# Kernel optimization log

Measured on AMD Instinct MI355X. Metric: run time of the kernel, lower is better.

Reference implementation:

```python
import jax, jax.numpy as jnp
import numpy as np

B, T, D_IN, P, Q, D_OUT = 128, 1024, 64, 128, 2, 64


def _lstm_layer(x, w_ih, w_hh, b):
    """One LSTM layer, batch_first. x: [B,T,Din], w_ih: [4P,Din], w_hh: [4P,P], b: [4P].
    PyTorch gate order: i, f, g, o."""
    # Precompute input contribution for all timesteps (the big, parallel GEMM).
    gx = jnp.einsum('btd,gd->btg', x, w_ih) + b          # [B,T,4P]
    gx_t = jnp.swapaxes(gx, 0, 1)                        # [T,B,4P] for scan
    p = w_hh.shape[1]
    h0 = jnp.zeros((x.shape[0], p), dtype=x.dtype)
    c0 = jnp.zeros((x.shape[0], p), dtype=x.dtype)

    def step(carry, g_in):
        h, c = carry
        g = g_in + h @ w_hh.T                            # [B,4P]
        i, f, gg, o = jnp.split(g, 4, axis=-1)
        i = jax.nn.sigmoid(i)
        f = jax.nn.sigmoid(f)
        gg = jnp.tanh(gg)
        o = jax.nn.sigmoid(o)
        c = f * c + i * gg
        h = o * jnp.tanh(c)
        return (h, c), h

    _, hs = jax.lax.scan(step, (h0, c0), gx_t)           # hs: [T,B,P]
    return jnp.swapaxes(hs, 0, 1)                        # [B,T,P]


def setup_inputs() -> dict:
    key = jax.random.key(0)
    ks = jax.random.split(key, 8)
    x = jax.random.normal(ks[0], (B, T, D_IN), dtype=jnp.float32)
    # weight_ih: kaiming-normal-ish; weight_hh: orthogonal-ish (random normal is a fine stand-in
    # numerically; init distribution doesn't change the math being tested).
    w_ih0 = jax.random.normal(ks[1], (4 * P, D_IN), dtype=jnp.float32) * (1.0 / np.sqrt(D_IN))
    w_hh0 = jax.random.normal(ks[2], (4 * P, P), dtype=jnp.float32) * (1.0 / np.sqrt(P))
    w_ih1 = jax.random.normal(ks[3], (4 * P, P), dtype=jnp.float32) * (1.0 / np.sqrt(P))
    w_hh1 = jax.random.normal(ks[4], (4 * P, P), dtype=jnp.float32) * (1.0 / np.sqrt(P))
    # biases initialized to zero in the original (bias_ih + bias_hh folded into one per layer
    # would be equivalent math; keep both for faithfulness)
    b_ih = jnp.zeros((Q, 4 * P), dtype=jnp.float32)
    b_hh = jnp.zeros((Q, 4 * P), dtype=jnp.float32)
    fc_w = jax.random.normal(ks[5], (D_OUT, P), dtype=jnp.float32) * np.sqrt(2.0 / P)
    fc_b = jnp.zeros((D_OUT,), dtype=jnp.float32)
    return {"x": x, "w_ih0": w_ih0, "w_hh0": w_hh0, "w_ih1": w_ih1, "w_hh1": w_hh1,
            "b_ih": b_ih, "b_hh": b_hh, "fc_w": fc_w, "fc_b": fc_b}


def reference(x, w_ih0, w_hh0, w_ih1, w_hh1, b_ih, b_hh, fc_w, fc_b):
    h = _lstm_layer(x, w_ih0, w_hh0, b_ih[0] + b_hh[0])   # layer 0: [B,T,P]
    h = _lstm_layer(h, w_ih1, w_hh1, b_ih[1] + b_hh[1])   # layer 1: [B,T,P]
    return jnp.einsum('btp,op->bto', h, fc_w) + fc_b      # [B,T,D_OUT]
```

## Files before the change

### kernel.cpp

```cpp
#include <hip/hip_runtime.h>

#define NT 1024
#define H0S 256
#define GS 64
#define LAG 32

typedef _Float16 half8 __attribute__((ext_vector_type(8)));
typedef _Float16 half4 __attribute__((ext_vector_type(4)));
typedef float f32x4 __attribute__((ext_vector_type(4)));
typedef unsigned long long u64;

#ifndef __has_builtin
#define __has_builtin(x) 0
#endif

__device__ __forceinline__ f32x4 MFMA(half8 a, half8 b, f32x4 c) {
  return __builtin_amdgcn_mfma_f32_16x16x32_f16(a, b, c, 0, 0, 0);
}
__device__ __forceinline__ float exp2h(float x) {
#if __has_builtin(__builtin_amdgcn_exp2f)
  return __builtin_amdgcn_exp2f(x);
#else
  return exp2f(x);
#endif
}
__device__ __forceinline__ float sigf(float x) {
  return __builtin_amdgcn_rcpf(1.0f + exp2h(x * -1.44269504f));
}
__device__ __forceinline__ float tanhf2(float x) {
  float t = __builtin_amdgcn_rcpf(1.0f + exp2h(x * 2.88539008f));
  return fmaf(-2.0f, t, 1.0f);
}
__device__ __forceinline__ half8 cvt8(float4 c0, float4 c1) {
  half8 hv;
  hv[0] = (_Float16)c0.x; hv[1] = (_Float16)c0.y;
  hv[2] = (_Float16)c0.z; hv[3] = (_Float16)c0.w;
  hv[4] = (_Float16)c1.x; hv[5] = (_Float16)c1.y;
  hv[6] = (_Float16)c1.z; hv[7] = (_Float16)c1.w;
  return hv;
}
__device__ __forceinline__ unsigned wpoll(unsigned* p, unsigned tgt,
                                          unsigned cached, int l) {
  unsigned c = cached;
  while (c < tgt) {
    unsigned pv = 0;
    if (l == 0)
      pv = __hip_atomic_load(p, __ATOMIC_ACQUIRE, __HIP_MEMORY_SCOPE_AGENT);
    c = (unsigned)__builtin_amdgcn_readfirstlane((int)pv);
    if (c < tgt) __builtin_amdgcn_s_sleep(2);
  }
  return c;
}

#define DRAIN_BARRIER()                              \
  asm volatile("s_waitcnt vmcnt(0)" ::: "memory");   \
  __builtin_amdgcn_sched_barrier(0);                 \
  __builtin_amdgcn_s_barrier();                      \
  __builtin_amdgcn_sched_barrier(0)

#define LGKM_BARRIER()                               \
  asm volatile("s_waitcnt lgkmcnt(0)" ::: "memory"); \
  __builtin_amdgcn_sched_barrier(0);                 \
  __builtin_amdgcn_s_barrier();                      \
  __builtin_amdgcn_sched_barrier(0)

__global__ __launch_bounds__(256) void prep_x(const float* __restrict__ x,
                                              _Float16* __restrict__ Xf) {
  int t0 = blockIdx.x * 256 + threadIdx.x;
  int l = t0 & 63;
  int fid = t0 >> 6;
  int kt = fid & 1;
  int t = (fid >> 1) & (NT - 1);
  int g = fid >> 11;
  int bt = g * 16 + (l & 15);
  int kb = kt * 32 + (l >> 4) * 4;
  const float* src = x + ((size_t)bt * NT + (size_t)t) * 64 + kb;
  float4 v0 = *(const float4*)src;
  float4 v1 = *(const float4*)(src + 16);
  *(half8*)(Xf + (size_t)fid * 512 + l * 8) = cvt8(v0, v1);
}

__global__ __launch_bounds__(512, 1) void lstm_main(
    const float* __restrict__ wih0, const float* __restrict__ whh0,
    const float* __restrict__ wih1, const float* __restrict__ whh1,
    const float* __restrict__ bih, const float* __restrict__ bhh,
    const float* __restrict__ fcw, const float* __restrict__ fcb,
    const _Float16* __restrict__ Xf, _Float16* __restrict__ h0R,
    float* __restrict__ gxR, float* __restrict__ gyR,
    unsigned* __restrict__ flags, float* __restrict__ out) {
  const int tid = threadIdx.x;
  const int w = tid >> 6, l = tid & 63;
  const int n = l & 15, lg = l >> 4;
  const int role = blockIdx.x >> 3;
  const int g = blockIdx.x & 7;

  __shared__ _Float16 hfr[2][4][64][8];

  _Float16* h0G = h0R + (size_t)g * H0S * 2048;
  float* gxG = gxR + (size_t)g * GS * 8192;
  float* gyG = gyR + (size_t)g * GS * 8192;
  unsigned* pX  = flags + (0 * 8 + g) * 16;
  unsigned* pXY = flags + (1 * 8 + g) * 16;
  unsigned* pP  = flags + (2 * 8 + g) * 16;
  unsigned* pY  = flags + (3 * 8 + g) * 16;
  const half8 hz = {0, 0, 0, 0, 0, 0, 0, 0};

  if (role == 0) {
    half8 Ax[4][2], Ai[4][4];
    f32x4 b0v[4], b1v[4];
#pragma unroll
    for (int q = 0; q < 4; ++q) {
      int row = (w + 8 * q) * 16 + n;
#pragma unroll
      for (int kt = 0; kt < 2; ++kt) {
        const float* wp = wih0 + (size_t)row * 64 + kt * 32 + lg * 4;
        Ax[q][kt] = cvt8(*(const float4*)wp, *(const float4*)(wp + 16));
      }
#pragma unroll
      for (int kt = 0; kt < 4; ++kt) {
        const float* wp = wih1 + (size_t)row * 128 + kt * 32 + lg * 4;
        Ai[q][kt] = cvt8(*(const float4*)wp, *(const float4*)(wp + 16));
      }
      int rb = (w + 8 * q) * 16 + lg * 4;
      f32x4 v0, v1;
#pragma unroll
      for (int r = 0; r < 4; ++r) {
        v0[r] = bih[rb + r] + bhh[rb + r];
        v1[r] = bih[512 + rb + r] + bhh[512 + rb + r];
      }
      b0v[q] = v0;
      b1v[q] = v1;
    }
    const _Float16* XfG = Xf + (size_t)g * NT * 1024;
    half8 xv0 = *(const half8*)(XfG + l * 8);
    half8 xv1 = *(const half8*)(XfG + 512 + l * 8);
    half8 hb0 = hz, hb1 = hz, hb2 = hz, hb3 = hz;
    unsigned Pp = 0, Yp = 0;
    for (int s = 0; s < NT + LAG; ++s) {
      const int u = s - LAG;
      if (s < NT) {
        f32x4 a0 = MFMA(Ax[0][0], xv0, b0v[0]);
        f32x4 a1 = MFMA(Ax[1][0], xv0, b0v[1]);
        f32x4 a2 = MFMA(Ax[2][0], xv0, b0v[2]);
        f32x4 a3 = MFMA(Ax[3][0], xv0, b0v[3]);
        a0 = MFMA(Ax[0][1], xv1, a0); a1 = MFMA(Ax[1][1], xv1, a1);
        a2 = MFMA(Ax[2][1], xv1, a2); a3 = MFMA(Ax[3][1], xv1, a3);
        float* gp = gxG + (size_t)(s & (GS - 1)) * 8192;
        *(f32x4*)(gp + ((0 + w) * 64 + l) * 4) = a0;
        *(f32x4*)(gp + ((8 + w) * 64 + l) * 4) = a1;
        *(f32x4*)(gp + ((16 + w) * 64 + l) * 4) = a2;
        *(f32x4*)(gp + ((24 + w) * 64 + l) * 4) = a3;
        if (s + 1 < NT) {
          const _Float16* p = XfG + (size_t)(s + 1) * 1024 + l * 8;
          xv0 = *(const half8*)p;
          xv1 = *(const half8*)(p + 512);
        }
      }
      if (u >= 0) {
        if (u == 0) {
          Pp = wpoll(pP, 1u, Pp, l);
          const _Float16* hp = h0G + l * 8;
          hb0 = *(const half8*)hp;
          hb1 = *(const half8*)(hp + 512);
          hb2 = *(const half8*)(hp + 1024);
          hb3 = *(const half8*)(hp + 1536);
        }
        f32x4 c0 = MFMA(Ai[0][0], hb0, b1v[0]);
        f32x4 c1 = MFMA(Ai[1][0], hb0, b1v[1]);
        f32x4 c2 = MFMA(Ai[2][0], hb0, b1v[2]);
        f32x4 c3 = MFMA(Ai[3][0], hb0, b1v[3]);
        c0 = MFMA(Ai[0][1], hb1, c0); c1 = MFMA(Ai[1][1], hb1, c1);
        c2 = MFMA(Ai[2][1], hb1, c2); c3 = MFMA(Ai[3][1], hb1, c3);
        c0 = MFMA(Ai[0][2], hb2, c0); c1 = MFMA(Ai[1][2], hb2, c1);
        c2 = MFMA(Ai[2][2], hb2, c2); c3 = MFMA(Ai[3][2], hb2, c3);
        c0 = MFMA(Ai[0][3], hb3, c0); c1 = MFMA(Ai[1][3], hb3, c1);
        c2 = MFMA(Ai[2][3], hb3, c2); c3 = MFMA(Ai[3][3], hb3, c3);
        float* gp = gyG + (size_t)(u & (GS - 1)) * 8192;
        *(f32x4*)(gp + ((0 + w) * 64 + l) * 4) = c0;
        *(f32x4*)(gp + ((8 + w) * 64 + l) * 4) = c1;
        *(f32x4*)(gp + ((16 + w) * 64 + l) * 4) = c2;
        *(f32x4*)(gp + ((24 + w) * 64 + l) * 4) = c3;
        if (u + 1 < NT) {
          Pp = wpoll(pP, (unsigned)(u + 2), Pp, l);
          const _Float16* hp =
              h0G + (size_t)((u + 1) & (H0S - 1)) * 2048 + l * 8;
          hb0 = *(const half8*)hp;
          hb1 = *(const half8*)(hp + 512);
          hb2 = *(const half8*)(hp + 1024);
          hb3 = *(const half8*)(hp + 1536);
        }
        if ((u & 15) == 0 && u >= 56)
          Yp = wpoll(pY, (unsigned)(u - 48), Yp, l);
      }
      if ((s & 7) == 7) {
        DRAIN_BARRIER();
        if (tid == 0) {
          __hip_atomic_store(pX, (unsigned)(s + 1), __ATOMIC_RELEASE,
                             __HIP_MEMORY_SCOPE_AGENT);
          if (u >= 0)
            __hip_atomic_store(pXY, (unsigned)(u + 1), __ATOMIC_RELEASE,
                               __HIP_MEMORY_SCOPE_AGENT);
        }
      }
    }
    DRAIN_BARRIER();
    if (tid == 0) {
      __hip_atomic_store(pX, (unsigned)(NT + LAG), __ATOMIC_RELEASE,
                         __HIP_MEMORY_SCOPE_AGENT);
      __hip_atomic_store(pXY, (unsigned)(NT + LAG), __ATOMIC_RELEASE,
                         __HIP_MEMORY_SCOPE_AGENT);
    }
  } else if (role == 1) {
    half8 Ah[4][4];
#pragma unroll
    for (int q = 0; q < 4; ++q) {
      int row = (w + 8 * q) * 16 + n;
#pragma unroll
      for (int kt = 0; kt < 4; ++kt) {
        const float* wp = whh0 + (size_t)row * 128 + kt * 32 + lg * 4;
        Ah[q][kt] = cvt8(*(const float4*)wp, *(const float4*)(wp + 16));
      }
    }
    if (tid < 256) ((half8*)&hfr[1][0][0][0])[tid] = hz;
    f32x4 cst = {0.f, 0.f, 0.f, 0.f};
    unsigned Xp = wpoll(pX, 2u, 0u, l);
    f32x4 gA0 = *(const f32x4*)(gxG + ((0 + w) * 64 + l) * 4);
    f32x4 gA1 = *(const f32x4*)(gxG + ((8 + w) * 64 + l) * 4);
    f32x4 gA2 = *(const f32x4*)(gxG + ((16 + w) * 64 + l) * 4);
    f32x4 gA3 = *(const f32x4*)(gxG + ((24 + w) * 64 + l) * 4);
    const float* g1 = gxG + 8192;
    f32x4 gB0 = *(const f32x4*)(g1 + ((0 + w) * 64 + l) * 4);
    f32x4 gB1 = *(const f32x4*)(g1 + ((8 + w) * 64 + l) * 4);
    f32x4 gB2 = *(const f32x4*)(g1 + ((16 + w) * 64 + l) * 4);
    f32x4 gB3 = *(const f32x4*)(g1 + ((24 + w) * 64 + l) * 4);
    __syncthreads();

#define PSTEP(T, G0, G1, G2, G3)                                               \
  {                                                                            \
    const int rdk_ = ((T) + 1) & 1;                                            \
    half8 b0 = *(const half8*)&hfr[rdk_][0][l][0];                             \
    half8 b1 = *(const half8*)&hfr[rdk_][1][l][0];                             \
    half8 b2 = *(const half8*)&hfr[rdk_][2][l][0];                             \
    half8 b3 = *(const half8*)&hfr[rdk_][3][l][0];                             \
    f32x4 c0 = G0, c1 = G1, c2 = G2, c3 = G3;                                  \
    c0 = MFMA(Ah[0][0], b0, c0); c1 = MFMA(Ah[1][0], b0, c1);                  \
    c2 = MFMA(Ah[2][0], b0, c2); c3 = MFMA(Ah[3][0], b0, c3);                  \
    c0 = MFMA(Ah[0][1], b1, c0); c1 = MFMA(Ah[1][1], b1, c1);                  \
    c2 = MFMA(Ah[2][1], b1, c2); c3 = MFMA(Ah[3][1], b1, c3);                  \
    c0 = MFMA(Ah[0][2], b2, c0); c1 = MFMA(Ah[1][2], b2, c1);                  \
    c2 = MFMA(Ah[2][2], b2, c2); c3 = MFMA(Ah[3][2], b2, c3);                  \
    c0 = MFMA(Ah[0][3], b3, c0); c1 = MFMA(Ah[1][3], b3, c1);                  \
    c2 = MFMA(Ah[2][3], b3, c2); c3 = MFMA(Ah[3][3], b3, c3);                  \
    if ((T) + 2 < NT) {      \
      Xp = wpoll(pX, (unsigned)((T) + 3), Xp, l);                              \
      const float* gp_ = gxG + (size_t)(((T) + 2) & (GS - 1)) * 8192;          \
      G0 = *(const f32x4*)(gp_ + ((0 + w) * 64 + l) * 4);                      \
      G1 = *(const f32x4*)(gp_ + ((8 + w) * 64 + l) * 4);                      \
      G2 = *(const f32x4*)(gp_ + ((16 + w) * 64 + l) * 4);                     \
      G3 = *(const f32x4*)(gp_ + ((24 + w) * 64 + l) * 4);                     \
    }                                                                          \
    half4 hh;                                                                  \
    _Pragma("unroll")                                                          \
    for (int r = 0; r < 4; ++r) {                                              \
      float iv = sigf(c0[r]), fv = sigf(c1[r]);                                \
      float gv = tanhf2(c2[r]), ov = sigf(c3[r]);                              \
      cst[r] = fv * cst[r] + iv * gv;                                          \
      hh[r] = (_Float16)(ov * tanhf2(cst[r]));                                 \
    }                                                                          \
    *(half4*)&hfr[(T) & 1][w >> 1][l][(w & 1) << 2] = hh;                      \
    *(u64*)(h0G + (size_t)((T) & (H0S - 1)) * 2048 + (w >> 1) * 512 + l * 8 +  \
            (w & 1) * 4) = __builtin_bit_cast(u64, hh);                        \
    LGKM_BARRIER();                                                            \
    if (((T) & 7) == 7) {                                                      \
      DRAIN_BARRIER();                                                         \
      if (tid == 0)                                                            \
        __hip_atomic_store(pP, (unsigned)((T) + 1), __ATOMIC_RELEASE,          \
                           __HIP_MEMORY_SCOPE_AGENT);                          \
    }                                                                          \
  }

    for (int s = 0; s < NT; s += 2) {
      PSTEP(s, gA0, gA1, gA2, gA3);
      PSTEP(s + 1, gB0, gB1, gB2, gB3);
    }
#undef PSTEP
  } else {
    half8 Ah[4][4], FCA[4];
    f32x4 fcbv = {0.f, 0.f, 0.f, 0.f};
#pragma unroll
    for (int q = 0; q < 4; ++q) {
      int row = (w + 8 * q) * 16 + n;
#pragma unroll
      for (int kt = 0; kt < 4; ++kt) {
        const float* wp = whh1 + (size_t)row * 128 + kt * 32 + lg * 4;
        Ah[q][kt] = cvt8(*(const float4*)wp, *(const float4*)(wp + 16));
      }
    }
    const bool fcon = (w < 4);
    if (fcon) {
      int frow = (w << 4) + n;
#pragma unroll
      for (int kt = 0; kt < 4; ++kt) {
        const float* wp = fcw + (size_t)frow * 128 + kt * 32 + lg * 4;
        FCA[kt] = cvt8(*(const float4*)wp, *(const float4*)(wp + 16));
      }
      fcbv = *(const f32x4*)(fcb + (w << 4) + lg * 4);
    }
    if (tid < 256) ((half8*)&hfr[1][0][0][0])[tid] = hz;
    float* outG = out + (size_t)((g << 4) + n) * NT * 64 + (w << 4) + lg * 4;
    f32x4 cst = {0.f, 0.f, 0.f, 0.f};
    unsigned XYp = wpoll(pXY, 2u, 0u, l);
    f32x4 gA0 = *(const f32x4*)(gyG + ((0 + w) * 64 + l) * 4);
    f32x4 gA1 = *(const f32x4*)(gyG + ((8 + w) * 64 + l) * 4);
    f32x4 gA2 = *(const f32x4*)(gyG + ((16 + w) * 64 + l) * 4);
    f32x4 gA3 = *(const f32x4*)(gyG + ((24 + w) * 64 + l) * 4);
    const float* g1 = gyG + 8192;
    f32x4 gB0 = *(const f32x4*)(g1 + ((0 + w) * 64 + l) * 4);
    f32x4 gB1 = *(const f32x4*)(g1 + ((8 + w) * 64 + l) * 4);
    f32x4 gB2 = *(const f32x4*)(g1 + ((16 + w) * 64 + l) * 4);
    f32x4 gB3 = *(const f32x4*)(g1 + ((24 + w) * 64 + l) * 4);
    __syncthreads();

#define YSTEP(T, G0, G1, G2, G3)                                               \
  {                                                                            \
    const int rdk_ = ((T) + 1) & 1;                                            \
    half8 b0 = *(const half8*)&hfr[rdk_][0][l][0];                             \
    half8 b1 = *(const half8*)&hfr[rdk_][1][l][0];                             \
    half8 b2 = *(const half8*)&hfr[rdk_][2][l][0];                             \
    half8 b3 = *(const half8*)&hfr[rdk_][3][l][0];                             \
    f32x4 c0 = G0, c1 = G1, c2 = G2, c3 = G3;                                  \
    c0 = MFMA(Ah[0][0], b0, c0); c1 = MFMA(Ah[1][0], b0, c1);                  \
    c2 = MFMA(Ah[2][0], b0, c2); c3 = MFMA(Ah[3][0], b0, c3);                  \
    c0 = MFMA(Ah[0][1], b1, c0); c1 = MFMA(Ah[1][1], b1, c1);                  \
    c2 = MFMA(Ah[2][1], b1, c2); c3 = MFMA(Ah[3][1], b1, c3);                  \
    c0 = MFMA(Ah[0][2], b2, c0); c1 = MFMA(Ah[1][2], b2, c1);                  \
    c2 = MFMA(Ah[2][2], b2, c2); c3 = MFMA(Ah[3][2], b2, c3);                  \
    c0 = MFMA(Ah[0][3], b3, c0); c1 = MFMA(Ah[1][3], b3, c1);                  \
    c2 = MFMA(Ah[2][3], b3, c2); c3 = MFMA(Ah[3][3], b3, c3);                  \
    if (fcon) {                                             \
      f32x4 afc = fcbv;                                                        \
      afc = MFMA(FCA[0], b0, afc); afc = MFMA(FCA[1], b1, afc);                \
      afc = MFMA(FCA[2], b2, afc); afc = MFMA(FCA[3], b3, afc);                \
      if ((T) >= 1) *(f32x4*)(outG + (size_t)((T) - 1) * 64) = afc;            \
    }                                                                          \
    if ((T) + 2 < NT) {                                  \
      XYp = wpoll(pXY, (unsigned)((T) + 3), XYp, l);                           \
      const float* gp_ = gyG + (size_t)(((T) + 2) & (GS - 1)) * 8192;          \
      G0 = *(const f32x4*)(gp_ + ((0 + w) * 64 + l) * 4);                      \
      G1 = *(const f32x4*)(gp_ + ((8 + w) * 64 + l) * 4);                      \
      G2 = *(const f32x4*)(gp_ + ((16 + w) * 64 + l) * 4);                     \
      G3 = *(const f32x4*)(gp_ + ((24 + w) * 64 + l) * 4);                     \
    }                                                                          \
    half4 hh;                                                                  \
    _Pragma("unroll")                                                          \
    for (int r = 0; r < 4; ++r) {                                              \
      float iv = sigf(c0[r]), fv = sigf(c1[r]);                                \
      float gv = tanhf2(c2[r]), ov = sigf(c3[r]);                              \
      cst[r] = fv * cst[r] + iv * gv;                                          \
      hh[r] = (_Float16)(ov * tanhf2(cst[r]));                                 \
    }                                                                          \
    *(half4*)&hfr[(T) & 1][w >> 1][l][(w & 1) << 2] = hh;                      \
    LGKM_BARRIER();                                                            \
    if (((T) & 7) == 7 && tid == 0)       \
      __hip_atomic_store(pY, (unsigned)((T) + 1), __ATOMIC_RELAXED,            \
                         __HIP_MEMORY_SCOPE_AGENT);                            \
  }

    for (int t = 0; t < NT; t += 2) {
      YSTEP(t, gA0, gA1, gA2, gA3);
      YSTEP(t + 1, gB0, gB1, gB2, gB3);
    }
#undef YSTEP
    {
      const int rdk = (NT + 1) & 1;
      half8 b0 = *(const half8*)&hfr[rdk][0][l][0];
      half8 b1 = *(const half8*)&hfr[rdk][1][l][0];
      half8 b2 = *(const half8*)&hfr[rdk][2][l][0];
      half8 b3 = *(const half8*)&hfr[rdk][3][l][0];
      if (fcon) {
        f32x4 afc = fcbv;
        afc = MFMA(FCA[0], b0, afc); afc = MFMA(FCA[1], b1, afc);
        afc = MFMA(FCA[2], b2, afc); afc = MFMA(FCA[3], b3, afc);
        *(f32x4*)(outG + (size_t)(NT - 1) * 64) = afc;
      }
    }
  }
}

extern "C" void kernel_launch(void* const* d_in, const int* in_sizes, int n_in,
                              void* d_out, int out_size, void* d_ws, size_t ws_size,
                              hipStream_t stream) {
  const float* x     = (const float*)d_in[0];
  const float* w_ih0 = (const float*)d_in[1];
  const float* w_hh0 = (const float*)d_in[2];
  const float* w_ih1 = (const float*)d_in[3];
  const float* w_hh1 = (const float*)d_in[4];
  const float* b_ih  = (const float*)d_in[5];
  const float* b_hh  = (const float*)d_in[6];
  const float* fc_w  = (const float*)d_in[7];
  const float* fc_b  = (const float*)d_in[8];

  _Float16* Xf  = (_Float16*)d_ws;
  _Float16* h0R = (_Float16*)((char*)d_ws + (16u << 20));
  float* gxR    = (float*)((char*)d_ws + (24u << 20));
  float* gyR    = (float*)((char*)d_ws + (40u << 20));
  unsigned* flags = (unsigned*)((char*)d_ws + (56u << 20));

  (void)hipMemsetAsync(flags, 0, 4096, stream);
  prep_x<<<4096, 256, 0, stream>>>(x, Xf);
  lstm_main<<<24, 512, 0, stream>>>(w_ih0, w_hh0, w_ih1, w_hh1, b_ih, b_hh,
                                    fc_w, fc_b, Xf, h0R, gxR, gyR, flags,
                                    (float*)d_out);
}
```

Baseline: 1.230 ms.

## Interleave two batch groups per recurrent block to hide per-step latency

Each recurrent-role block (layer-0 and layer-1) now processes two independent 16-sample batch groups, interleaving their MFMA chains and gate math within one timestep. The grid shrinks from 24 to 16 blocks. The intent is to fill the dependent-chain latency of one group's MFMAs and transcendentals with the other group's independent work, since the per-step cost is dominated by latency rather than throughput. In exchange each step does twice the work per block, and register pressure rises, which could lengthen the serial critical path.

```diff
diff --git a/kernel.cpp b/kernel.cpp
--- a/kernel.cpp
+++ b/kernel.cpp
@@ -63,6 +63,16 @@
   __builtin_amdgcn_sched_barrier(0);                 \
   __builtin_amdgcn_s_barrier();                      \
   __builtin_amdgcn_sched_barrier(0)
+
+#define HHCHAIN(Ah, b0, b1, b2, b3, c0, c1, c2, c3)                            \
+  c0 = MFMA(Ah[0][0], b0, c0); c1 = MFMA(Ah[1][0], b0, c1);                    \
+  c2 = MFMA(Ah[2][0], b0, c2); c3 = MFMA(Ah[3][0], b0, c3);                    \
+  c0 = MFMA(Ah[0][1], b1, c0); c1 = MFMA(Ah[1][1], b1, c1);                    \
+  c2 = MFMA(Ah[2][1], b1, c2); c3 = MFMA(Ah[3][1], b1, c3);                    \
+  c0 = MFMA(Ah[0][2], b2, c0); c1 = MFMA(Ah[1][2], b2, c1);                    \
+  c2 = MFMA(Ah[2][2], b2, c2); c3 = MFMA(Ah[3][2], b2, c3);                    \
+  c0 = MFMA(Ah[0][3], b3, c0); c1 = MFMA(Ah[1][3], b3, c1);                    \
+  c2 = MFMA(Ah[2][3], b3, c2); c3 = MFMA(Ah[3][3], b3, c3)
 
 __global__ __launch_bounds__(256) void prep_x(const float* __restrict__ x,
                                               _Float16* __restrict__ Xf) {
@@ -91,21 +101,20 @@
   const int tid = threadIdx.x;
   const int w = tid >> 6, l = tid & 63;
   const int n = l & 15, lg = l >> 4;
-  const int role = blockIdx.x >> 3;
-  const int g = blockIdx.x & 7;
-
-  __shared__ _Float16 hfr[2][4][64][8];
-
-  _Float16* h0G = h0R + (size_t)g * H0S * 2048;
-  float* gxG = gxR + (size_t)g * GS * 8192;
-  float* gyG = gyR + (size_t)g * GS * 8192;
-  unsigned* pX  = flags + (0 * 8 + g) * 16;
-  unsigned* pXY = flags + (1 * 8 + g) * 16;
-  unsigned* pP  = flags + (2 * 8 + g) * 16;
-  unsigned* pY  = flags + (3 * 8 + g) * 16;
+
+  __shared__ _Float16 hfr[2][2][4][64][8];
   const half8 hz = {0, 0, 0, 0, 0, 0, 0, 0};
 
-  if (role == 0) {
+  if (blockIdx.x < 8) {
+    const int g = blockIdx.x;
+    _Float16* h0G = h0R + (size_t)g * H0S * 2048;
+    float* gxG = gxR + (size_t)g * GS * 8192;
+    float* gyG = gyR + (size_t)g * GS * 8192;
+    unsigned* pX  = flags + (0 * 8 + g) * 16;
+    unsigned* pXY = flags + (1 * 8 + g) * 16;
+    unsigned* pP  = flags + (2 * 8 + g) * 16;
+    unsigned* pY  = flags + (3 * 8 + g) * 16;
+
     half8 Ax[4][2], Ai[4][4];
     f32x4 b0v[4], b1v[4];
 #pragma unroll
@@ -210,7 +219,17 @@
       __hip_atomic_store(pXY, (unsigned)(NT + LAG), __ATOMIC_RELEASE,
                          __HIP_MEMORY_SCOPE_AGENT);
     }
-  } else if (role == 1) {
+  } else if (blockIdx.x < 12) {
+    const int gA = (blockIdx.x - 8) * 2, gB = gA + 1;
+    _Float16* h0A = h0R + (size_t)gA * H0S * 2048;
+    _Float16* h0B = h0R + (size_t)gB * H0S * 2048;
+    float* gxA = gxR + (size_t)gA * GS * 8192;
+    float* gxB = gxR + (size_t)gB * GS * 8192;
+    unsigned* pXA = flags + (0 * 8 + gA) * 16;
+    unsigned* pXB = flags + (0 * 8 + gB) * 16;
+    unsigned* pPA = flags + (2 * 8 + gA) * 16;
+    unsigned* pPB = flags + (2 * 8 + gB) * 16;
+
     half8 Ah[4][4];
 #pragma unroll
     for (int q = 0; q < 4; ++q) {
@@ -221,70 +240,109 @@
         Ah[q][kt] = cvt8(*(const float4*)wp, *(const float4*)(wp + 16));
       }
     }
-    if (tid < 256) ((half8*)&hfr[1][0][0][0])[tid] = hz;
-    f32x4 cst = {0.f, 0.f, 0.f, 0.f};
-    unsigned Xp = wpoll(pX, 2u, 0u, l);
-    f32x4 gA0 = *(const f32x4*)(gxG + ((0 + w) * 64 + l) * 4);
-    f32x4 gA1 = *(const f32x4*)(gxG + ((8 + w) * 64 + l) * 4);
-    f32x4 gA2 = *(const f32x4*)(gxG + ((16 + w) * 64 + l) * 4);
-    f32x4 gA3 = *(const f32x4*)(gxG + ((24 + w) * 64 + l) * 4);
-    const float* g1 = gxG + 8192;
-    f32x4 gB0 = *(const f32x4*)(g1 + ((0 + w) * 64 + l) * 4);
-    f32x4 gB1 = *(const f32x4*)(g1 + ((8 + w) * 64 + l) * 4);
-    f32x4 gB2 = *(const f32x4*)(g1 + ((16 + w) * 64 + l) * 4);
-    f32x4 gB3 = *(const f32x4*)(g1 + ((24 + w) * 64 + l) * 4);
+    {
+      int grp = tid >> 8, idx = tid & 255;
+      ((half8*)&hfr[grp][1][0][0][0])[idx] = hz;
+    }
+    f32x4 cstA = {0.f, 0.f, 0.f, 0.f}, cstB = {0.f, 0.f, 0.f, 0.f};
+    unsigned XpA = wpoll(pXA, 2u, 0u, l);
+    unsigned XpB = wpoll(pXB, 2u, 0u, l);
+    f32x4 gAa0 = *(const f32x4*)(gxA + ((0 + w) * 64 + l) * 4);
+    f32x4 gAa1 = *(const f32x4*)(gxA + ((8 + w) * 64 + l) * 4);
+    f32x4 gAa2 = *(const f32x4*)(gxA + ((16 + w) * 64 + l) * 4);
+    f32x4 gAa3 = *(const f32x4*)(gxA + ((24 + w) * 64 + l) * 4);
+    f32x4 gBa0 = *(const f32x4*)(gxB + ((0 + w) * 64 + l) * 4);
+    f32x4 gBa1 = *(const f32x4*)(gxB + ((8 + w) * 64 + l) * 4);
+    f32x4 gBa2 = *(const f32x4*)(gxB + ((16 + w) * 64 + l) * 4);
+    f32x4 gBa3 = *(const f32x4*)(gxB + ((24 + w) * 64 + l) * 4);
+    const float* gA1p = gxA + 8192;
+    const float* gB1p = gxB + 8192;
+    f32x4 gAb0 = *(const f32x4*)(gA1p + ((0 + w) * 64 + l) * 4);
+    f32x4 gAb1 = *(const f32x4*)(gA1p + ((8 + w) * 64 + l) * 4);
+    f32x4 gAb2 = *(const f32x4*)(gA1p + ((16 + w) * 64 + l) * 4);
+    f32x4 gAb3 = *(const f32x4*)(gA1p + ((24 + w) * 64 + l) * 4);
+    f32x4 gBb0 = *(const f32x4*)(gB1p + ((0 + w) * 64 + l) * 4);
+    f32x4 gBb1 = *(const f32x4*)(gB1p + ((8 + w) * 64 + l) * 4);
+    f32x4 gBb2 = *(const f32x4*)(gB1p + ((16 + w) * 64 + l) * 4);
+    f32x4 gBb3 = *(const f32x4*)(gB1p + ((24 + w) * 64 + l) * 4);
     __syncthreads();
 
-#define PSTEP(T, G0, G1, G2, G3)                                               \
+#define PSTEP(T, QA0, QA1, QA2, QA3, QB0, QB1, QB2, QB3)                       \
   {                                                                            \
     const int rdk_ = ((T) + 1) & 1;                                            \
-    half8 b0 = *(const half8*)&hfr[rdk_][0][l][0];                             \
-    half8 b1 = *(const half8*)&hfr[rdk_][1][l][0];                             \
-    half8 b2 = *(const half8*)&hfr[rdk_][2][l][0];                             \
-    half8 b3 = *(const half8*)&hfr[rdk_][3][l][0];                             \
-    f32x4 c0 = G0, c1 = G1, c2 = G2, c3 = G3;                                  \
-    c0 = MFMA(Ah[0][0], b0, c0); c1 = MFMA(Ah[1][0], b0, c1);                  \
-    c2 = MFMA(Ah[2][0], b0, c2); c3 = MFMA(Ah[3][0], b0, c3);                  \
-    c0 = MFMA(Ah[0][1], b1, c0); c1 = MFMA(Ah[1][1], b1, c1);                  \
-    c2 = MFMA(Ah[2][1], b1, c2); c3 = MFMA(Ah[3][1], b1, c3);                  \
-    c0 = MFMA(Ah[0][2], b2, c0); c1 = MFMA(Ah[1][2], b2, c1);                  \
-    c2 = MFMA(Ah[2][2], b2, c2); c3 = MFMA(Ah[3][2], b2, c3);                  \
-    c0 = MFMA(Ah[0][3], b3, c0); c1 = MFMA(Ah[1][3], b3, c1);                  \
-    c2 = MFMA(Ah[2][3], b3, c2); c3 = MFMA(Ah[3][3], b3, c3);                  \
-    if ((T) + 2 < NT) {      \
-      Xp = wpoll(pX, (unsigned)((T) + 3), Xp, l);                              \
-      const float* gp_ = gxG + (size_t)(((T) + 2) & (GS - 1)) * 8192;          \
-      G0 = *(const f32x4*)(gp_ + ((0 + w) * 64 + l) * 4);                      \
-      G1 = *(const f32x4*)(gp_ + ((8 + w) * 64 + l) * 4);                      \
-      G2 = *(const f32x4*)(gp_ + ((16 + w) * 64 + l) * 4);                     \
-      G3 = *(const f32x4*)(gp_ + ((24 + w) * 64 + l) * 4);                     \
-    }                                                                          \
-    half4 hh;                                                                  \
+    half8 a0 = *(const half8*)&hfr[0][rdk_][0][l][0];                          \
+    half8 a1 = *(const half8*)&hfr[0][rdk_][1][l][0];                          \
+    half8 a2 = *(const half8*)&hfr[0][rdk_][2][l][0];                          \
+    half8 a3 = *(const half8*)&hfr[0][rdk_][3][l][0];                          \
+    half8 e0 = *(const half8*)&hfr[1][rdk_][0][l][0];                          \
+    half8 e1 = *(const half8*)&hfr[1][rdk_][1][l][0];                          \
+    half8 e2 = *(const half8*)&hfr[1][rdk_][2][l][0];                          \
+    half8 e3 = *(const half8*)&hfr[1][rdk_][3][l][0];                          \
+    f32x4 cA0 = QA0, cA1 = QA1, cA2 = QA2, cA3 = QA3;                          \
+    f32x4 cB0 = QB0, cB1 = QB1, cB2 = QB2, cB3 = QB3;                          \
+    HHCHAIN(Ah, a0, a1, a2, a3, cA0, cA1, cA2, cA3);                           \
+    HHCHAIN(Ah, e0, e1, e2, e3, cB0, cB1, cB2, cB3);                           \
+    if ((T) + 2 < NT) {                                                        \
+      XpA = wpoll(pXA, (unsigned)((T) + 3), XpA, l);                           \
+      XpB = wpoll(pXB, (unsigned)((T) + 3), XpB, l);                           \
+      const float* pa_ = gxA + (size_t)(((T) + 2) & (GS - 1)) * 8192;          \
+      const float* pb_ = gxB + (size_t)(((T) + 2) & (GS - 1)) * 8192;          \
+      QA0 = *(const f32x4*)(pa_ + ((0 + w) * 64 + l) * 4);                     \
+      QA1 = *(const f32x4*)(pa_ + ((8 + w) * 64 + l) * 4);                     \
+      QA2 = *(const f32x4*)(pa_ + ((16 + w) * 64 + l) * 4);                    \
+      QA3 = *(const f32x4*)(pa_ + ((24 + w) * 64 + l) * 4);                    \
+      QB0 = *(const f32x4*)(pb_ + ((0 + w) * 64 + l) * 4);                     \
+      QB1 = *(const f32x4*)(pb_ + ((8 + w) * 64 + l) * 4);                     \
+      QB2 = *(const f32x4*)(pb_ + ((16 + w) * 64 + l) * 4);                    \
+      QB3 = *(const f32x4*)(pb_ + ((24 + w) * 64 + l) * 4);                    \
+    }                                                                          \
+    half4 hhA, hhB;                                                            \
     _Pragma("unroll")                                                          \
     for (int r = 0; r < 4; ++r) {                                              \
-      float iv = sigf(c0[r]), fv = sigf(c1[r]);                                \
-      float gv = tanhf2(c2[r]), ov = sigf(c3[r]);                              \
-      cst[r] = fv * cst[r] + iv * gv;                                          \
-      hh[r] = (_Float16)(ov * tanhf2(cst[r]));                                 \
-    }                                                                          \
-    *(half4*)&hfr[(T) & 1][w >> 1][l][(w & 1) << 2] = hh;                      \
-    *(u64*)(h0G + (size_t)((T) & (H0S - 1)) * 2048 + (w >> 1) * 512 + l * 8 +  \
-            (w & 1) * 4) = __builtin_bit_cast(u64, hh);                        \
+      float iv = sigf(cA0[r]), fv = sigf(cA1[r]);                              \
+      float gv = tanhf2(cA2[r]), ov = sigf(cA3[r]);                            \
+      cstA[r] = fv * cstA[r] + iv * gv;                                        \
+      hhA[r] = (_Float16)(ov * tanhf2(cstA[r]));                               \
+    }                                                                          \
+    _Pragma("unroll")                                                          \
+    for (int r = 0; r < 4; ++r) {                                              \
+      float iv = sigf(cB0[r]), fv = sigf(cB1[r]);                              \
+      float gv = tanhf2(cB2[r]), ov = sigf(cB3[r]);                            \
+      cstB[r] = fv * cstB[r] + iv * gv;                                        \
+      hhB[r] = (_Float16)(ov * tanhf2(cstB[r]));                               \
+    }                                                                          \
+    *(half4*)&hfr[0][(T) & 1][w >> 1][l][(w & 1) << 2] = hhA;                  \
+    *(half4*)&hfr[1][(T) & 1][w >> 1][l][(w & 1) << 2] = hhB;                  \
+    *(u64*)(h0A + (size_t)((T) & (H0S - 1)) * 2048 + (w >> 1) * 512 + l * 8 +  \
+            (w & 1) * 4) = __builtin_bit_cast(u64, hhA);                       \
+    *(u64*)(h0B + (size_t)((T) & (H0S - 1)) * 2048 + (w >> 1) * 512 + l * 8 +  \
+            (w & 1) * 4) = __builtin_bit_cast(u64, hhB);                       \
     LGKM_BARRIER();                                                            \
     if (((T) & 7) == 7) {                                                      \
       DRAIN_BARRIER();                                                         \
-      if (tid == 0)                                                            \
-        __hip_atomic_store(pP, (unsigned)((T) + 1), __ATOMIC_RELEASE,          \
+      if (tid == 0) {                                                          \
+        __hip_atomic_store(pPA, (unsigned)((T) + 1), __ATOMIC_RELEASE,         \
                            __HIP_MEMORY_SCOPE_AGENT);                          \
+        __hip_atomic_store(pPB, (unsigned)((T) + 1), __ATOMIC_RELEASE,         \
+                           __HIP_MEMORY_SCOPE_AGENT);                          \
+      }                                                                        \
     }                                                                          \
   }
 
     for (int s = 0; s < NT; s += 2) {
-      PSTEP(s, gA0, gA1, gA2, gA3);
-      PSTEP(s + 1, gB0, gB1, gB2, gB3);
+      PSTEP(s, gAa0, gAa1, gAa2, gAa3, gBa0, gBa1, gBa2, gBa3);
+      PSTEP(s + 1, gAb0, gAb1, gAb2, gAb3, gBb0, gBb1, gBb2, gBb3);
     }
 #undef PSTEP
   } else {
+    const int gA = (blockIdx.x - 12) * 2, gB = gA + 1;
+    float* gyA = gyR + (size_t)gA * GS * 8192;
+    float* gyB = gyR + (size_t)gB * GS * 8192;
+    unsigned* pXYA = flags + (1 * 8 + gA) * 16;
+    unsigned* pXYB = flags + (1 * 8 + gB) * 16;
+    unsigned* pYA = flags + (3 * 8 + gA) * 16;
+    unsigned* pYB = flags + (3 * 8 + gB) * 16;
+
     half8 Ah[4][4], FCA[4];
     f32x4 fcbv = {0.f, 0.f, 0.f, 0.f};
 #pragma unroll
@@ -306,82 +364,124 @@
       }
       fcbv = *(const f32x4*)(fcb + (w << 4) + lg * 4);
     }
-    if (tid < 256) ((half8*)&hfr[1][0][0][0])[tid] = hz;
-    float* outG = out + (size_t)((g << 4) + n) * NT * 64 + (w << 4) + lg * 4;
-    f32x4 cst = {0.f, 0.f, 0.f, 0.f};
-    unsigned XYp = wpoll(pXY, 2u, 0u, l);
-    f32x4 gA0 = *(const f32x4*)(gyG + ((0 + w) * 64 + l) * 4);
-    f32x4 gA1 = *(const f32x4*)(gyG + ((8 + w) * 64 + l) * 4);
-    f32x4 gA2 = *(const f32x4*)(gyG + ((16 + w) * 64 + l) * 4);
-    f32x4 gA3 = *(const f32x4*)(gyG + ((24 + w) * 64 + l) * 4);
-    const float* g1 = gyG + 8192;
-    f32x4 gB0 = *(const f32x4*)(g1 + ((0 + w) * 64 + l) * 4);
-    f32x4 gB1 = *(const f32x4*)(g1 + ((8 + w) * 64 + l) * 4);
-    f32x4 gB2 = *(const f32x4*)(g1 + ((16 + w) * 64 + l) * 4);
-    f32x4 gB3 = *(const f32x4*)(g1 + ((24 + w) * 64 + l) * 4);
+    {
+      int grp = tid >> 8, idx = tid & 255;
+      ((half8*)&hfr[grp][1][0][0][0])[idx] = hz;
+    }
+    float* outA = out + (size_t)((gA << 4) + n) * NT * 64 + (w << 4) + lg * 4;
+    float* outB = out + (size_t)((gB << 4) + n) * NT * 64 + (w << 4) + lg * 4;
+    f32x4 cstA = {0.f, 0.f, 0.f, 0.f}, cstB = {0.f, 0.f, 0.f, 0.f};
+    unsigned XpA = wpoll(pXYA, 2u, 0u, l);
+    unsigned XpB = wpoll(pXYB, 2u, 0u, l);
+    f32x4 gAa0 = *(const f32x4*)(gyA + ((0 + w) * 64 + l) * 4);
+    f32x4 gAa1 = *(const f32x4*)(gyA + ((8 + w) * 64 + l) * 4);
+    f32x4 gAa2 = *(const f32x4*)(gyA + ((16 + w) * 64 + l) * 4);
+    f32x4 gAa3 = *(const f32x4*)(gyA + ((24 + w) * 64 + l) * 4);
+    f32x4 gBa0 = *(const f32x4*)(gyB + ((0 + w) * 64 + l) * 4);
+    f32x4 gBa1 = *(const f32x4*)(gyB + ((8 + w) * 64 + l) * 4);
+    f32x4 gBa2 = *(const f32x4*)(gyB + ((16 + w) * 64 + l) * 4);
+    f32x4 gBa3 = *(const f32x4*)(gyB + ((24 + w) * 64 + l) * 4);
+    const float* gA1p = gyA + 8192;
+    const float* gB1p = gyB + 8192;
+    f32x4 gAb0 = *(const f32x4*)(gA1p + ((0 + w) * 64 + l) * 4);
+    f32x4 gAb1 = *(const f32x4*)(gA1p + ((8 + w) * 64 + l) * 4);
+    f32x4 gAb2 = *(const f32x4*)(gA1p + ((16 + w) * 64 + l) * 4);
+    f32x4 gAb3 = *(const f32x4*)(gA1p + ((24 + w) * 64 + l) * 4);
+    f32x4 gBb0 = *(const f32x4*)(gB1p + ((0 + w) * 64 + l) * 4);
+    f32x4 gBb1 = *(const f32x4*)(gB1p + ((8 + w) * 64 + l) * 4);
+    f32x4 gBb2 = *(const f32x4*)(gB1p + ((16 + w) * 64 + l) * 4);
+    f32x4 gBb3 = *(const f32x4*)(gB1p + ((24 + w) * 64 + l) * 4);
     __syncthreads();
 
-#define YSTEP(T, G0, G1, G2, G3)                                               \
+#define YSTEP(T, QA0, QA1, QA2, QA3, QB0, QB1, QB2, QB3)                       \
   {                                                                            \
     const int rdk_ = ((T) + 1) & 1;                                            \
-    half8 b0 = *(const half8*)&hfr[rdk_][0][l][0];                             \
-    half8 b1 = *(const half8*)&hfr[rdk_][1][l][0];                             \
-    half8 b2 = *(const half8*)&hfr[rdk_][2][l][0];                             \
-    half8 b3 = *(const half8*)&hfr[rdk_][3][l][0];                             \
-    f32x4 c0 = G0, c1 = G1, c2 = G2, c3 = G3;                                  \
-    c0 = MFMA(Ah[0][0], b0, c0); c1 = MFMA(Ah[1][0], b0, c1);                  \
-    c2 = MFMA(Ah[2][0], b0, c2); c3 = MFMA(Ah[3][0], b0, c3);                  \
-    c0 = MFMA(Ah[0][1], b1, c0); c1 = MFMA(Ah[1][1], b1, c1);                  \
-    c2 = MFMA(Ah[2][1], b1, c2); c3 = MFMA(Ah[3][1], b1, c3);                  \
-    c0 = MFMA(Ah[0][2], b2, c0); c1 = MFMA(Ah[1][2], b2, c1);                  \
-    c2 = MFMA(Ah[2][2], b2, c2); c3 = MFMA(Ah[3][2], b2, c3);                  \
-    c0 = MFMA(Ah[0][3], b3, c0); c1 = MFMA(Ah[1][3], b3, c1);                  \
-    c2 = MFMA(Ah[2][3], b3, c2); c3 = MFMA(Ah[3][3], b3, c3);                  \
-    if (fcon) {                                             \
-      f32x4 afc = fcbv;                                                        \
-      afc = MFMA(FCA[0], b0, afc); afc = MFMA(FCA[1], b1, afc);                \
-      afc = MFMA(FCA[2], b2, afc); afc = MFMA(FCA[3], b3, afc);                \
-      if ((T) >= 1) *(f32x4*)(outG + (size_t)((T) - 1) * 64) = afc;            \
-    }                                                                          \
-    if ((T) + 2 < NT) {                                  \
-      XYp = wpoll(pXY, (unsigned)((T) + 3), XYp, l);                           \
-      const float* gp_ = gyG + (size_t)(((T) + 2) & (GS - 1)) * 8192;          \
-      G0 = *(const f32x4*)(gp_ + ((0 + w) * 64 + l) * 4);                      \
-      G1 = *(const f32x4*)(gp_ + ((8 + w) * 64 + l) * 4);                      \
-      G2 = *(const f32x4*)(gp_ + ((16 + w) * 64 + l) * 4);                     \
-      G3 = *(const f32x4*)(gp_ + ((24 + w) * 64 + l) * 4);                     \
-    }                                                                          \
-    half4 hh;                                                                  \
+    half8 a0 = *(const half8*)&hfr[0][rdk_][0][l][0];                          \
+    half8 a1 = *(const half8*)&hfr[0][rdk_][1][l][0];                          \
+    half8 a2 = *(const half8*)&hfr[0][rdk_][2][l][0];                          \
+    half8 a3 = *(const half8*)&hfr[0][rdk_][3][l][0];                          \
+    half8 e0 = *(const half8*)&hfr[1][rdk_][0][l][0];                          \
+    half8 e1 = *(const half8*)&hfr[1][rdk_][1][l][0];                          \
+    half8 e2 = *(const half8*)&hfr[1][rdk_][2][l][0];                          \
+    half8 e3 = *(const half8*)&hfr[1][rdk_][3][l][0];                          \
+    f32x4 cA0 = QA0, cA1 = QA1, cA2 = QA2, cA3 = QA3;                          \
+    f32x4 cB0 = QB0, cB1 = QB1, cB2 = QB2, cB3 = QB3;                          \
+    HHCHAIN(Ah, a0, a1, a2, a3, cA0, cA1, cA2, cA3);                           \
+    HHCHAIN(Ah, e0, e1, e2, e3, cB0, cB1, cB2, cB3);                           \
+    if (fcon) {                                \
+      f32x4 afcA = fcbv, afcB = fcbv;                                          \
+      afcA = MFMA(FCA[0], a0, afcA); afcA = MFMA(FCA[1], a1, afcA);            \
+      afcA = MFMA(FCA[2], a2, afcA); afcA = MFMA(FCA[3], a3, afcA);            \
+      afcB = MFMA(FCA[0], e0, afcB); afcB = MFMA(FCA[1], e1, afcB);            \
+      afcB = MFMA(FCA[2], e2, afcB); afcB = MFMA(FCA[3], e3, afcB);            \
+      if ((T) >= 1) {                                                          \
+        *(f32x4*)(outA + (size_t)((T) - 1) * 64) = afcA;                       \
+        *(f32x4*)(outB + (size_t)((T) - 1) * 64) = afcB;                       \
+      }                                                                        \
+    }                                                                          \
+    if ((T) + 2 < NT) {                                                        \
+      XpA = wpoll(pXYA, (unsigned)((T) + 3), XpA, l);                          \
+      XpB = wpoll(pXYB, (unsigned)((T) + 3), XpB, l);                          \
+      const float* pa_ = gyA + (size_t)(((T) + 2) & (GS - 1)) * 8192;          \
+      const float* pb_ = gyB + (size_t)(((T) + 2) & (GS - 1)) * 8192;          \
+      QA0 = *(const f32x4*)(pa_ + ((0 + w) * 64 + l) * 4);                     \
+      QA1 = *(const f32x4*)(pa_ + ((8 + w) * 64 + l) * 4);                     \
+      QA2 = *(const f32x4*)(pa_ + ((16 + w) * 64 + l) * 4);                    \
+      QA3 = *(const f32x4*)(pa_ + ((24 + w) * 64 + l) * 4);                    \
+      QB0 = *(const f32x4*)(pb_ + ((0 + w) * 64 + l) * 4);                     \
+      QB1 = *(const f32x4*)(pb_ + ((8 + w) * 64 + l) * 4);                     \
+      QB2 = *(const f32x4*)(pb_ + ((16 + w) * 64 + l) * 4);                    \
+      QB3 = *(const f32x4*)(pb_ + ((24 + w) * 64 + l) * 4);                    \
+    }                                                                          \
+    half4 hhA, hhB;                                                            \
     _Pragma("unroll")                                                          \
     for (int r = 0; r < 4; ++r) {                                              \
-      float iv = sigf(c0[r]), fv = sigf(c1[r]);                                \
-      float gv = tanhf2(c2[r]), ov = sigf(c3[r]);                              \
-      cst[r] = fv * cst[r] + iv * gv;                                          \
-      hh[r] = (_Float16)(ov * tanhf2(cst[r]));                                 \
-    }                                                                          \
-    *(half4*)&hfr[(T) & 1][w >> 1][l][(w & 1) << 2] = hh;                      \
+      float iv = sigf(cA0[r]), fv = sigf(cA1[r]);                              \
+      float gv = tanhf2(cA2[r]), ov = sigf(cA3[r]);                            \
+      cstA[r] = fv * cstA[r] + iv * gv;                                        \
+      hhA[r] = (_Float16)(ov * tanhf2(cstA[r]));                               \
+    }                                                                          \
+    _Pragma("unroll")                                                          \
+    for (int r = 0; r < 4; ++r) {                                              \
+      float iv = sigf(cB0[r]), fv = sigf(cB1[r]);                              \
+      float gv = tanhf2(cB2[r]), ov = sigf(cB3[r]);                            \
+      cstB[r] = fv * cstB[r] + iv * gv;                                        \
+      hhB[r] = (_Float16)(ov * tanhf2(cstB[r]));                               \
+    }                                                                          \
+    *(half4*)&hfr[0][(T) & 1][w >> 1][l][(w & 1) << 2] = hhA;                  \
+    *(half4*)&hfr[1][(T) & 1][w >> 1][l][(w & 1) << 2] = hhB;                  \
     LGKM_BARRIER();                                                            \
-    if (((T) & 7) == 7 && tid == 0)       \
-      __hip_atomic_store(pY, (unsigned)((T) + 1), __ATOMIC_RELAXED,            \
+    if (((T) & 7) == 7 && tid == 0) {                                          \
+      __hip_atomic_store(pYA, (unsigned)((T) + 1), __ATOMIC_RELAXED,           \
                          __HIP_MEMORY_SCOPE_AGENT);                            \
+      __hip_atomic_store(pYB, (unsigned)((T) + 1), __ATOMIC_RELAXED,           \
+                         __HIP_MEMORY_SCOPE_AGENT);                            \
+    }                                                                          \
   }
 
     for (int t = 0; t < NT; t += 2) {
-      YSTEP(t, gA0, gA1, gA2, gA3);
-      YSTEP(t + 1, gB0, gB1, gB2, gB3);
+      YSTEP(t, gAa0, gAa1, gAa2, gAa3, gBa0, gBa1, gBa2, gBa3);
+      YSTEP(t + 1, gAb0, gAb1, gAb2, gAb3, gBb0, gBb1, gBb2, gBb3);
     }
 #undef YSTEP
     {
       const int rdk = (NT + 1) & 1;
-      half8 b0 = *(const half8*)&hfr[rdk][0][l][0];
-      half8 b1 = *(const half8*)&hfr[rdk][1][l][0];
-      half8 b2 = *(const half8*)&hfr[rdk][2][l][0];
-      half8 b3 = *(const half8*)&hfr[rdk][3][l][0];
+      half8 a0 = *(const half8*)&hfr[0][rdk][0][l][0];
+      half8 a1 = *(const half8*)&hfr[0][rdk][1][l][0];
+      half8 a2 = *(const half8*)&hfr[0][rdk][2][l][0];
+      half8 a3 = *(const half8*)&hfr[0][rdk][3][l][0];
+      half8 e0 = *(const half8*)&hfr[1][rdk][0][l][0];
+      half8 e1 = *(const half8*)&hfr[1][rdk][1][l][0];
+      half8 e2 = *(const half8*)&hfr[1][rdk][2][l][0];
+      half8 e3 = *(const half8*)&hfr[1][rdk][3][l][0];
       if (fcon) {
-        f32x4 afc = fcbv;
-        afc = MFMA(FCA[0], b0, afc); afc = MFMA(FCA[1], b1, afc);
-        afc = MFMA(FCA[2], b2, afc); afc = MFMA(FCA[3], b3, afc);
-        *(f32x4*)(outG + (size_t)(NT - 1) * 64) = afc;
+        f32x4 afcA = fcbv, afcB = fcbv;
+        afcA = MFMA(FCA[0], a0, afcA); afcA = MFMA(FCA[1], a1, afcA);
+        afcA = MFMA(FCA[2], a2, afcA); afcA = MFMA(FCA[3], a3, afcA);
+        afcB = MFMA(FCA[0], e0, afcB); afcB = MFMA(FCA[1], e1, afcB);
+        afcB = MFMA(FCA[2], e2, afcB); afcB = MFMA(FCA[3], e3, afcB);
+        *(f32x4*)(outA + (size_t)(NT - 1) * 64) = afcA;
+        *(f32x4*)(outB + (size_t)(NT - 1) * 64) = afcB;
       }
     }
   }
@@ -408,7 +508,7 @@
 
   (void)hipMemsetAsync(flags, 0, 4096, stream);
   prep_x<<<4096, 256, 0, stream>>>(x, Xf);
-  lstm_main<<<24, 512, 0, stream>>>(w_ih0, w_hh0, w_ih1, w_hh1, b_ih, b_hh,
+  lstm_main<<<16, 512, 0, stream>>>(w_ih0, w_hh0, w_ih1, w_hh1, b_ih, b_hh,
                                     fc_w, fc_b, Xf, h0R, gxR, gyR, flags,
                                     (float*)d_out);
 }
```

Result: slower. 1.869 ms (+52.0%).
